# Kernel optimization log

Measured on AMD Instinct MI355X. Metric: run time of the kernel, lower is better.

The kernel has to match this reference:

```python
import jax, jax.numpy as jnp
import numpy as np

LN_EPS = 1e-9

def _layer_norm(x, g, b):
    mu = jnp.mean(x, axis=-1, keepdims=True)
    var = jnp.mean((x - mu) ** 2, axis=-1, keepdims=True)
    return (x - mu) * jax.lax.rsqrt(var + LN_EPS) * g + b

def _ffn(x, w1, b1, w2, b2, ln_g, ln_b):
    h = jax.nn.gelu(x @ w1 + b1, approximate=False)
    h = h @ w2 + b2
    return _layer_norm(h, ln_g, ln_b)

def _kernel_mean(x, y):
    d = x.shape[1]
    x2 = jnp.sum(x * x, axis=1)[:, None]
    y2 = jnp.sum(y * y, axis=1)[None, :]
    sq = x2 + y2 - 2.0 * (x @ y.T)  # [Nx, Ny]
    return jnp.mean(jnp.exp(-sq / (d * d)))

def _mmd(x, y):
    return _kernel_mean(x, x) + _kernel_mean(y, y) - 2.0 * _kernel_mean(x, y)

def setup_inputs() -> dict:
    key = jax.random.key(0)
    ks = jax.random.split(key, 8)
    B, S, D, DI, DL = 8, 512, 1024, 4096, 64
    s = lambda fan: 1.0 / np.sqrt(fan)
    return {
        "hidden": jax.random.normal(ks[0], (B, S, D), jnp.float32),
        "true_samples": jax.random.normal(ks[1], (B * S, DL), jnp.float32),
        "enc_w1": jax.random.normal(ks[2], (D, DI), jnp.float32) * s(D),
        "enc_b1": jnp.zeros((DI,), jnp.float32),
        "enc_w2": jax.random.normal(ks[3], (DI, DL), jnp.float32) * s(DI),
        "enc_b2": jnp.zeros((DL,), jnp.float32),
        "enc_ln_g": jnp.ones((DL,), jnp.float32),
        "enc_ln_b": jnp.zeros((DL,), jnp.float32),
        "dec_w1": jax.random.normal(ks[4], (DL, DI), jnp.float32) * s(DL),
        "dec_b1": jnp.zeros((DI,), jnp.float32),
        "dec_w2": jax.random.normal(ks[5], (DI, D), jnp.float32) * s(DI),
        "dec_b2": jnp.zeros((D,), jnp.float32),
        "dec_ln_g": jnp.ones((D,), jnp.float32),
        "dec_ln_b": jnp.zeros((D,), jnp.float32),
    }

def reference(hidden, true_samples, enc_w1, enc_b1, enc_w2, enc_b2, enc_ln_g, enc_ln_b,
              dec_w1, dec_b1, dec_w2, dec_b2, dec_ln_g, dec_ln_b):
    latent = _ffn(hidden, enc_w1, enc_b1, enc_w2, enc_b2, enc_ln_g, enc_ln_b)  # [B,S,DL]
    recon = _ffn(latent, dec_w1, dec_b1, dec_w2, dec_b2, dec_ln_g, dec_ln_b)   # [B,S,D]
    B, S, DL = latent.shape
    lat_flat = latent.reshape(-1, DL)  # [B*S, DL]
    reg_loss = _mmd(true_samples, lat_flat) / B * S
    return recon, latent, reg_loss
```

## Files before the change

### kernel.cpp

```cpp
#include <hip/hip_runtime.h>
#include <hip/hip_bf16.h>
#include <math.h>


typedef __attribute__((ext_vector_type(8))) short short8;
typedef __attribute__((ext_vector_type(4))) float float4a;
typedef __attribute__((ext_vector_type(4))) unsigned short us4;

__device__ inline ushort bf16r(float x) {
    union { float f; unsigned u; } c; c.f = x;
    unsigned r = (c.u + 0x7fffu + ((c.u >> 16) & 1u)) >> 16;
    return (ushort)r;
}

__device__ inline void gld_lds16(const void* g, void* l) {
    __builtin_amdgcn_global_load_lds(
        (const __attribute__((address_space(1))) void*)g,
        (__attribute__((address_space(3))) void*)l, 16, 0, 0);
}

template <int N> __device__ inline void wait_vmcnt() {
    if constexpr (N == 0) asm volatile("s_waitcnt vmcnt(0)" ::: "memory");
    else if constexpr (N == 4) asm volatile("s_waitcnt vmcnt(4)" ::: "memory");
    else if constexpr (N == 6) asm volatile("s_waitcnt vmcnt(6)" ::: "memory");
}

template <int N> __device__ inline void wait_lgkmcnt() {
    if constexpr (N == 0) asm volatile("s_waitcnt lgkmcnt(0)" ::: "memory");
    else if constexpr (N == 2) asm volatile("s_waitcnt lgkmcnt(2)" ::: "memory");
    else if constexpr (N == 4) asm volatile("s_waitcnt lgkmcnt(4)" ::: "memory");
    else if constexpr (N == 6) asm volatile("s_waitcnt lgkmcnt(6)" ::: "memory");
    else if constexpr (N == 8) asm volatile("s_waitcnt lgkmcnt(8)" ::: "memory");
}

__device__ inline void wait_lgkm_dyn(int n) {
    if (n == 0) wait_lgkmcnt<0>();
    else if (n == 2) wait_lgkmcnt<2>();
    else if (n == 4) wait_lgkmcnt<4>();
    else if (n == 6) wait_lgkmcnt<6>();
    else wait_lgkmcnt<8>();
}

__device__ inline float fast_gelu(float v) {
    float v2 = v * v;
    float u = v * __builtin_fmaf(0.07135481627f, v2, 1.5957691216f);
    u = fminf(u, 30.0f);
    float e = __expf(u);
    return v * e * __builtin_amdgcn_rcpf(e + 1.0f);
}

__global__ __launch_bounds__(256) void k_pre(
        const float* __restrict__ hidden, ushort* __restrict__ A1bf,
        const float* __restrict__ tsamp, ushort* __restrict__ Tbf,
        float* __restrict__ sq_t, float* __restrict__ acc,
        const float* __restrict__ i0, ushort* __restrict__ o0,
        const float* __restrict__ i1, ushort* __restrict__ o1,
        const float* __restrict__ i2, ushort* __restrict__ o2,
        const float* __restrict__ i3, ushort* __restrict__ o3) {
    int b = blockIdx.x, tid = threadIdx.x;
    if (b == 0 && tid < 24) acc[tid] = 0.0f;
    if (b < 4096) {
        int i = b * 1024 + tid * 4;
        float4 v = *(const float4*)(hidden + i);
        us4 o = {bf16r(v.x), bf16r(v.y), bf16r(v.z), bf16r(v.w)};
        *(us4*)(A1bf + i) = o;
        return;
    }
    if (b < 4352) {
        int i = (b - 4096) * 1024 + tid * 4;
        float4 v = *(const float4*)(tsamp + i);
        us4 o = {bf16r(v.x), bf16r(v.y), bf16r(v.z), bf16r(v.w)};
        *(us4*)(Tbf + i) = o;
        float s = v.x * v.x + v.y * v.y + v.z * v.z + v.w * v.w;
#pragma unroll
        for (int off = 8; off; off >>= 1) s += __shfl_xor(s, off);
        if ((tid & 15) == 0) sq_t[i >> 6] = s;
        return;
    }
    __shared__ float t[32][33];
    const float* in; ushort* out; int R, C, lb;
    if (b < 8448)      { in = i0; out = o0; R = 1024; C = 4096; lb = b - 4352; }
    else if (b < 8704) { in = i1; out = o1; R = 4096; C = 64;   lb = b - 8448; }
    else if (b < 8960) { in = i2; out = o2; R = 64;   C = 4096; lb = b - 8704; }
    else               { in = i3; out = o3; R = 4096; C = 1024; lb = b - 8960; }
    int bx = (lb % (C / 32)) * 32;
    int by = (lb / (C / 32)) * 32;
    int tx = tid & 31, ty = tid >> 5;
#pragma unroll
    for (int i = 0; i < 32; i += 8)
        t[ty + i][tx] = in[(size_t)(by + ty + i) * C + (bx + tx)];
    __syncthreads();
#pragma unroll
    for (int i = 0; i < 32; i += 8)
        out[(size_t)(bx + ty + i) * R + (by + tx)] = bf16r(t[tx][ty + i]);
}

template <int BN, int EPI, bool SWZ>
__global__ __launch_bounds__(256) void k_gemm(
        const ushort* __restrict__ A, const ushort* __restrict__ Bt,
        const float* __restrict__ bias, void* __restrict__ Out,
        float* __restrict__ Out2, int M, int N, int K, int KC) {
    constexpr int BM = 128, BK = 64;
    constexpr int WAVES_N = BN / 64;
    constexpr int WAVES_M = 4 / WAVES_N;
    constexpr int WM = BM / WAVES_M;
    constexpr int MT = WM / 16;
    constexpr int NT = 4;
    constexpr int CA = BM / 32, CB = BN / 32;

    __shared__ ushort sA[BM * 64];
    __shared__ ushort sB[BN * 64];

    const int tid  = threadIdx.x;
    const int wave = tid >> 6, lane = tid & 63;
    const int wm = wave / WAVES_N, wn = wave % WAVES_N;
    int bx = blockIdx.x, by = blockIdx.y;
    if constexpr (SWZ) {
        int lin = blockIdx.x + gridDim.x * blockIdx.y;
        by = lin % gridDim.y;
        bx = lin / gridDim.y;
    }
    const int m0 = by * BM, n0 = bx * BN;
    const int lrow = lane & 15, lq = lane >> 4;
    const int srow8 = lane >> 3;
    const int sk8   = lane & 7;
    const int kbeg = blockIdx.z * KC;

    const ushort* pA[CA]; unsigned lA[CA];
#pragma unroll
    for (int j = 0; j < CA; ++j) {
        int c = wave * CA + j;
        int r = c * 8 + srow8;
        pA[j] = &A[(size_t)(m0 + r) * K + kbeg + ((sk8 ^ (r & 7)) * 8)];
        lA[j] = c * 512;
    }
    const ushort* pB[CB]; unsigned lB[CB];
#pragma unroll
    for (int j = 0; j < CB; ++j) {
        int c = wave * CB + j;
        int r = c * 8 + srow8;
        pB[j] = &Bt[(size_t)(n0 + r) * K + kbeg + ((sk8 ^ (r & 7)) * 8)];
        lB[j] = c * 512;
    }
    unsigned aoff[2][MT], boff[2][NT];
#pragma unroll
    for (int h = 0; h < 2; ++h) {
#pragma unroll
        for (int mt = 0; mt < MT; ++mt) {
            int r = wm * WM + mt * 16 + lrow;
            aoff[h][mt] = r * 64 + (((h * 4 + lq) ^ (r & 7)) * 8);
        }
#pragma unroll
        for (int nt = 0; nt < NT; ++nt) {
            int r = wn * 64 + nt * 16 + lrow;
            boff[h][nt] = r * 64 + (((h * 4 + lq) ^ (r & 7)) * 8);
        }
    }

    float4a acc[MT][NT];
#pragma unroll
    for (int mt = 0; mt < MT; ++mt)
#pragma unroll
        for (int nt = 0; nt < NT; ++nt)
            acc[mt][nt] = (float4a){0.f, 0.f, 0.f, 0.f};

    for (int k0 = 0; k0 < KC; k0 += BK) {
#pragma unroll
        for (int j = 0; j < CA; ++j) {
            gld_lds16(pA[j], &sA[lA[j]]);
            pA[j] += BK;
        }
#pragma unroll
        for (int j = 0; j < CB; ++j) {
            gld_lds16(pB[j], &sB[lB[j]]);
            pB[j] += BK;
        }
        __syncthreads();
#pragma unroll
        for (int h = 0; h < 2; ++h) {
            short8 af[MT], bfr[NT];
#pragma unroll
            for (int mt = 0; mt < MT; ++mt)
                af[mt] = *(short8*)(&sA[aoff[h][mt]]);
#pragma unroll
            for (int nt = 0; nt < NT; ++nt)
                bfr[nt] = *(short8*)(&sB[boff[h][nt]]);
#pragma unroll
            for (int mt = 0; mt < MT; ++mt)
#pragma unroll
                for (int nt = 0; nt < NT; ++nt)
                    acc[mt][nt] = __builtin_amdgcn_mfma_f32_16x16x32_bf16(
                        af[mt], bfr[nt], acc[mt][nt], 0, 0, 0);
        }
        __syncthreads();
    }

    float* dstp = nullptr;
    if constexpr (EPI == 2) {
        if (Out2 && blockIdx.z) dstp = Out2;
        else dstp = (float*)Out + (size_t)blockIdx.z * M * N;
    }
#pragma unroll
    for (int mt = 0; mt < MT; ++mt)
#pragma unroll
        for (int nt = 0; nt < NT; ++nt) {
            int col = n0 + wn * 64 + nt * 16 + lrow;
            float bv = 0.f;
            if constexpr (EPI != 2) bv = bias[col];
#pragma unroll
            for (int r = 0; r < 4; ++r) {
                int row = m0 + wm * WM + mt * 16 + lq * 4 + r;
                float v = acc[mt][nt][r] + bv;
                if constexpr (EPI == 0) {
                    ((ushort*)Out)[(size_t)row * N + col] = bf16r(fast_gelu(v));
                } else if constexpr (EPI == 1) {
                    ((float*)Out)[(size_t)row * N + col] = v;
                } else {
                    dstp[(size_t)row * N + col] = v;
                }
            }
        }
}

template <int BN, int EPI, int CX, int CY>
__global__ __launch_bounds__(512, 2) void k_gemm256(
        const ushort* __restrict__ A, const ushort* __restrict__ Bt,
        const float* __restrict__ bias, void* __restrict__ Out,
        float* __restrict__ Out2, int M, int N, int K, int KC) {
    constexpr int BM = 256, BK = 64;
    constexpr int AI = 4;
    constexpr int BI = BN / 64;
    constexpr int WAVES_N = BN / 64;
    constexpr int WAVES_M = 8 / WAVES_N;
    constexpr int WM = BM / WAVES_M;
    constexpr int MT = WM / 16;
    constexpr int NT = 4;
    constexpr int NS = MT;
    constexpr int NS2 = MT / 2;

    __shared__ ushort sA[2][BM * 64];
    __shared__ ushort sB[2][BN * 64];

    const int tid = threadIdx.x;
    const int wave = tid >> 6, lane = tid & 63;
    const int wm = wave / WAVES_N, wn = wave % WAVES_N;

    const int gx = gridDim.x, gy = gridDim.y;
    const int lin = blockIdx.x + gx * (blockIdx.y + gy * blockIdx.z);
    const int nwg = gx * gy * gridDim.z;
    const int cpx = nwg >> 3;
    const int swz = (lin & 7) * cpx + (lin >> 3);
    const int nz  = gx * gy;
    const int zz  = swz / nz;
    const int rr  = swz % nz;
    const int chunk = rr / (CX * CY);
    const int lcl   = rr % (CX * CY);
    const int ncx   = gx / CX;
    const int bx = (chunk % ncx) * CX + (lcl % CX);
    const int by = (chunk / ncx) * CY + (lcl / CX);

    const int m0 = by * BM, n0 = bx * BN;
    const int lrow = lane & 15, lq = lane >> 4;
    const int kbeg = zz * KC;
    const int nT = KC / BK;

    const int crow = tid >> 3;
    const int ck8  = (tid & 7) ^ (crow & 7);
    const ushort* pAbase = A  + (size_t)(m0 + crow) * K + kbeg + ck8 * 8;
    const ushort* pBbase = Bt + (size_t)(n0 + crow) * K + kbeg + ck8 * 8;

    const int a0  = (wm * WM + lrow) * 64;
    const int b0  = (wn * 64 + lrow) * 64;
    const int sw0 = ((lq) ^ (lrow & 7)) * 8;
    const int sw1 = ((4 + lq) ^ (lrow & 7)) * 8;

    float4a acc[MT][NT];
#pragma unroll
    for (int mt = 0; mt < MT; ++mt)
#pragma unroll
        for (int nt = 0; nt < NT; ++nt)
            acc[mt][nt] = (float4a){0.f, 0.f, 0.f, 0.f};

#pragma unroll
    for (int j = 0; j < AI; ++j)
        gld_lds16(pAbase + (size_t)j * 64 * K, &sA[0][j * 4096 + wave * 512]);
#pragma unroll
    for (int j = 0; j < BI; ++j)
        gld_lds16(pBbase + (size_t)j * 64 * K, &sB[0][j * 4096 + wave * 512]);
    wait_vmcnt<0>();
    __builtin_amdgcn_s_barrier();
    __builtin_amdgcn_sched_barrier(0);

    for (int t = 0; t < nT; ++t) {
        const int d = t & 1;
        const bool pf1 = (t + 1 < nT);
        const size_t koff1 = (size_t)(t + 1) * BK;

        short8 af[NS][2], bfr[2][NT];

#pragma unroll
        for (int nt = 0; nt < NT; ++nt)
            bfr[0][nt] = *(const short8*)(&sB[d][b0 + nt * 1024 + sw0]);
        af[0][0] = *(const short8*)(&sA[d][a0 + 0 * 1024 + sw0]);
        af[0][1] = *(const short8*)(&sA[d][a0 + 1 * 1024 + sw0]);
        __builtin_amdgcn_sched_barrier(0);
        af[1][0] = *(const short8*)(&sA[d][a0 + 2 * 1024 + sw0]);
        af[1][1] = *(const short8*)(&sA[d][a0 + 3 * 1024 + sw0]);
        __builtin_amdgcn_sched_barrier(0);
        if (pf1) {
#pragma unroll
            for (int j = 0; j < AI; ++j)
                gld_lds16(pAbase + (size_t)j * 64 * K + koff1,
                          &sA[d ^ 1][j * 4096 + wave * 512]);
#pragma unroll
            for (int j = 0; j < BI; ++j)
                gld_lds16(pBbase + (size_t)j * 64 * K + koff1,
                          &sB[d ^ 1][j * 4096 + wave * 512]);
        }
        __builtin_amdgcn_sched_barrier(0);

#pragma unroll
        for (int s = 0; s < NS; ++s) {
            const int s2 = s + 2;
            if (s2 < NS) {
                const int h2 = s2 / NS2;
                const int mb2 = (s2 % NS2) * 2;
                const int swh2 = h2 ? sw1 : sw0;
                if ((s2 % NS2) == 0) {
#pragma unroll
                    for (int nt = 0; nt < NT; ++nt)
                        bfr[h2][nt] =
                            *(const short8*)(&sB[d][b0 + nt * 1024 + swh2]);
                }
                af[s2][0] = *(const short8*)(&sA[d][a0 + (mb2 + 0) * 1024 + swh2]);
                af[s2][1] = *(const short8*)(&sA[d][a0 + (mb2 + 1) * 1024 + swh2]);
                __builtin_amdgcn_sched_barrier(0);
            }
            int Ns = 0;
            if (s + 1 < NS) Ns += (((s + 1) % NS2) == 0) ? (2 + NT) : 2;
            if (s + 2 < NS) Ns += (((s + 2) % NS2) == 0) ? (2 + NT) : 2;
            wait_lgkm_dyn(Ns);
            __builtin_amdgcn_sched_barrier(0);
            const int h = s / NS2, mb = (s % NS2) * 2;
            __builtin_amdgcn_s_setprio(1);
#pragma unroll
            for (int i = 0; i < 2; ++i)
#pragma unroll
                for (int nt = 0; nt < NT; ++nt)
                    acc[mb + i][nt] = __builtin_amdgcn_mfma_f32_16x16x32_bf16(
                        af[s][i], bfr[h][nt], acc[mb + i][nt], 0, 0, 0);
            __builtin_amdgcn_s_setprio(0);
        }
        if (pf1) {
            wait_vmcnt<0>();
            __builtin_amdgcn_s_barrier();
            __builtin_amdgcn_sched_barrier(0);
        }
    }

    float* dstp = nullptr;
    if constexpr (EPI == 2) {
        if (Out2 && zz) dstp = Out2;
        else dstp = (float*)Out + (size_t)zz * M * N;
    }
#pragma unroll
    for (int mt = 0; mt < MT; ++mt)
#pragma unroll
        for (int nt = 0; nt < NT; ++nt) {
            const int col = n0 + wn * 64 + nt * 16 + lrow;
            float bv = 0.f;
            if constexpr (EPI == 0) bv = bias[col];
#pragma unroll
            for (int r = 0; r < 4; ++r) {
                const int row = m0 + wm * WM + mt * 16 + lq * 4 + r;
                float v = acc[mt][nt][r] + bv;
                if constexpr (EPI == 0)
                    ((ushort*)Out)[(size_t)row * N + col] = bf16r(fast_gelu(v));
                else
                    dstp[(size_t)row * N + col] = v;
            }
        }
}

__global__ __launch_bounds__(256) void k_gram_all(
        const ushort* __restrict__ Tbf, const ushort* __restrict__ Lbf,
        const float* __restrict__ sq_t, const float* __restrict__ sq_l,
        float* __restrict__ accum) {
    __shared__ ushort sX[128 * 64];
    __shared__ ushort sY[128 * 64];
    __shared__ float red[4];

    int id = blockIdx.x;
    int pair, tbx, tby; float w;
    if (id < 1056) {
        pair = (id < 528) ? 0 : 1;
        int t = (pair == 0) ? id : id - 528;
        int r = (int)((sqrtf(8.0f * t + 1.0f) - 1.0f) * 0.5f);
        while ((r + 1) * (r + 2) / 2 <= t) ++r;
        while (r * (r + 1) / 2 > t) --r;
        tby = r; tbx = t - r * (r + 1) / 2;
        w = (tbx == tby) ? 1.0f : 2.0f;
    } else {
        pair = 2; int t = id - 1056;
        tbx = t & 31; tby = t >> 5; w = 1.0f;
    }
    const ushort* Xb = (pair == 1) ? Lbf : Tbf;
    const ushort* Yb = (pair == 0) ? Tbf : Lbf;
    const float* sqX = (pair == 1) ? sq_l : sq_t;
    const float* sqY = (pair == 0) ? sq_t : sq_l;

    const int tid  = threadIdx.x;
    const int wave = tid >> 6, lane = tid & 63;
    const int wm = wave >> 1, wn = wave & 1;
    const int bx = tbx * 128, by = tby * 128;
    const int lrow = lane & 15, lq = lane >> 4;
    const int srow8 = lane >> 3, sk8 = lane & 7;

#pragma unroll
    for (int j = 0; j < 4; ++j) {
        int c = wave * 4 + j;
        int r = c * 8 + srow8;
        int kc = (sk8 ^ (r & 7)) * 8;
        gld_lds16(&Xb[(size_t)(bx + r) * 64 + kc], &sX[c * 512]);
        gld_lds16(&Yb[(size_t)(by + r) * 64 + kc], &sY[c * 512]);
    }

    unsigned xoff[2][4], yoff[2][4];
#pragma unroll
    for (int h = 0; h < 2; ++h)
#pragma unroll
        for (int i = 0; i < 4; ++i) {
            int rx = wm * 64 + i * 16 + lrow;
            int ry = wn * 64 + i * 16 + lrow;
            xoff[h][i] = rx * 64 + (((h * 4 + lq) ^ (rx & 7)) * 8);
            yoff[h][i] = ry * 64 + (((h * 4 + lq) ^ (ry & 7)) * 8);
        }
    __syncthreads();

    float4a acc[4][4];
#pragma unroll
    for (int mt = 0; mt < 4; ++mt)
#pragma unroll
        for (int nt = 0; nt < 4; ++nt)
            acc[mt][nt] = (float4a){0.f, 0.f, 0.f, 0.f};

#pragma unroll
    for (int h = 0; h < 2; ++h) {
        short8 xf[4], yf[4];
#pragma unroll
        for (int mt = 0; mt < 4; ++mt)
            xf[mt] = *(short8*)(&sX[xoff[h][mt]]);
#pragma unroll
        for (int nt = 0; nt < 4; ++nt)
            yf[nt] = *(short8*)(&sY[yoff[h][nt]]);
#pragma unroll
        for (int mt = 0; mt < 4; ++mt)
#pragma unroll
            for (int nt = 0; nt < 4; ++nt)
                acc[mt][nt] = __builtin_amdgcn_mfma_f32_16x16x32_bf16(
                    xf[mt], yf[nt], acc[mt][nt], 0, 0, 0);
    }

    float sy[4];
#pragma unroll
    for (int nt = 0; nt < 4; ++nt)
        sy[nt] = sqY[by + wn * 64 + nt * 16 + lrow];
    float s = 0.f;
#pragma unroll
    for (int mt = 0; mt < 4; ++mt)
#pragma unroll
        for (int r = 0; r < 4; ++r) {
            float sx = sqX[bx + wm * 64 + mt * 16 + lq * 4 + r];
#pragma unroll
            for (int nt = 0; nt < 4; ++nt)
                s += __expf((2.0f * acc[mt][nt][r] - sx - sy[nt]) * (1.0f / 4096.0f));
        }
    s *= w;
#pragma unroll
    for (int off = 32; off; off >>= 1) s += __shfl_xor(s, off);
    if ((tid & 63) == 0) red[tid >> 6] = s;
    __syncthreads();
    if (tid == 0) atomicAdd(accum + pair * 8, red[0] + red[1] + red[2] + red[3]);
}

__global__ __launch_bounds__(256) void k_ln64_red(
        const float* __restrict__ part, int npart,
        const float* __restrict__ bias, const float* __restrict__ g,
        const float* __restrict__ b, float* __restrict__ outf,
        ushort* __restrict__ outb, float* __restrict__ sq_l) {
    int wave = threadIdx.x >> 6, lane = threadIdx.x & 63;
    int row = blockIdx.x * 4 + wave;
    float x = bias[lane];
    for (int s = 0; s < npart; ++s)
        x += part[(size_t)s * 4096 * 64 + row * 64 + lane];
    float s = x;
#pragma unroll
    for (int off = 32; off; off >>= 1) s += __shfl_xor(s, off);
    float mu = s * (1.0f / 64.0f);
    float d = x - mu;
    float v = d * d;
#pragma unroll
    for (int off = 32; off; off >>= 1) v += __shfl_xor(v, off);
    float rs = rsqrtf(v * (1.0f / 64.0f) + 1e-9f);
    float y = d * rs * g[lane] + b[lane];
    outf[row * 64 + lane] = y;
    outb[row * 64 + lane] = bf16r(y);
    float q = y * y;
#pragma unroll
    for (int off = 32; off; off >>= 1) q += __shfl_xor(q, off);
    if (lane == 0) sq_l[row] = q;
}

__global__ __launch_bounds__(256) void k_ln1024_red(
        const float* __restrict__ p0, const float* __restrict__ p1,
        const float* __restrict__ bias, const float* __restrict__ g,
        const float* __restrict__ b, float* __restrict__ out) {
    __shared__ float red[4];
    int row = blockIdx.x, tid = threadIdx.x;
    const float4 v0 = *(const float4*)(p0 + (size_t)row * 1024 + tid * 4);
    const float4 v1 = *(const float4*)(p1 + (size_t)row * 1024 + tid * 4);
    const float4 bb = *(const float4*)(bias + tid * 4);
    float4 v;
    v.x = v0.x + v1.x + bb.x;
    v.y = v0.y + v1.y + bb.y;
    v.z = v0.z + v1.z + bb.z;
    v.w = v0.w + v1.w + bb.w;
    float s = v.x + v.y + v.z + v.w;
#pragma unroll
    for (int off = 32; off; off >>= 1) s += __shfl_xor(s, off);
    if ((tid & 63) == 0) red[tid >> 6] = s;
    __syncthreads();
    float mu = (red[0] + red[1] + red[2] + red[3]) * (1.0f / 1024.0f);
    float dx = v.x - mu, dy = v.y - mu, dz = v.z - mu, dw = v.w - mu;
    float q = dx * dx + dy * dy + dz * dz + dw * dw;
#pragma unroll
    for (int off = 32; off; off >>= 1) q += __shfl_xor(q, off);
    __syncthreads();
    if ((tid & 63) == 0) red[tid >> 6] = q;
    __syncthreads();
    float rs = rsqrtf((red[0] + red[1] + red[2] + red[3]) * (1.0f / 1024.0f) + 1e-9f);
    const float4 gv = *(const float4*)(g + tid * 4);
    const float4 bv = *(const float4*)(b + tid * 4);
    float4 o;
    o.x = dx * rs * gv.x + bv.x;
    o.y = dy * rs * gv.y + bv.y;
    o.z = dz * rs * gv.z + bv.z;
    o.w = dw * rs * gv.w + bv.w;
    *(float4*)(out + (size_t)row * 1024 + tid * 4) = o;
}

__global__ void k_finalize(const float* __restrict__ accum, float* __restrict__ out) {
    out[0] = (accum[0] + accum[8] - 2.0f * accum[16]) * (64.0f / (4096.0f * 4096.0f));
}

extern "C" void kernel_launch(void* const* d_in, const int* in_sizes, int n_in,
                              void* d_out, int out_size, void* d_ws, size_t ws_size,
                              hipStream_t stream) {
    const float* hidden   = (const float*)d_in[0];
    const float* tsamp    = (const float*)d_in[1];
    const float* enc_w1   = (const float*)d_in[2];
    const float* enc_b1   = (const float*)d_in[3];
    const float* enc_w2   = (const float*)d_in[4];
    const float* enc_b2   = (const float*)d_in[5];
    const float* enc_ln_g = (const float*)d_in[6];
    const float* enc_ln_b = (const float*)d_in[7];
    const float* dec_w1   = (const float*)d_in[8];
    const float* dec_b1   = (const float*)d_in[9];
    const float* dec_w2   = (const float*)d_in[10];
    const float* dec_b2   = (const float*)d_in[11];
    const float* dec_ln_g = (const float*)d_in[12];
    const float* dec_ln_b = (const float*)d_in[13];

    float* out      = (float*)d_out;
    float* recon    = out;
    float* latent_f = out + 4194304;
    float* reg      = out + 4456448;

    char* ws = (char*)d_ws;
    const size_t MB = 1024 * 1024;
    ushort* A1bf = (ushort*)(ws + 0);
    ushort* W1t  = (ushort*)(ws + 8 * MB);
    float*  part = (float*)(ws + 0);
    float*  h4p0 = (float*)(ws + 0);
    ushort* H1bf = (ushort*)(ws + 16 * MB);
    ushort* W4t  = (ushort*)(ws + 48 * MB);
    ushort* W2t  = (ushort*)(ws + 56 * MB);
    ushort* W3t  = (ushort*)(ws + 56 * MB + 512 * 1024);
    ushort* Lbf  = (ushort*)(ws + 57 * MB);
    float*  sq_t = (float*)(ws + 59 * MB);
    float*  sq_l = (float*)(ws + 59 * MB + 16384);
    float*  acc3 = (float*)(ws + 59 * MB + 32768);
    ushort* Tbf  = (ushort*)(ws + 59 * MB + 65536);

    k_pre<<<13056, 256, 0, stream>>>(hidden, A1bf, tsamp, Tbf, sq_t, acc3,
                                     enc_w1, W1t, enc_w2, W2t,
                                     dec_w1, W3t, dec_w2, W4t);

    k_gemm256<128, 0, 8, 4><<<dim3(32, 16, 1), 512, 0, stream>>>(
        A1bf, W1t, enc_b1, H1bf, nullptr, 4096, 4096, 1024, 1024);
    k_gemm<64, 2, false><<<dim3(1, 32, 16), 256, 0, stream>>>(
        H1bf, W2t, nullptr, part, nullptr, 4096, 64, 4096, 256);
    k_ln64_red<<<1024, 256, 0, stream>>>(part, 16, enc_b2, enc_ln_g, enc_ln_b,
                                         latent_f, Lbf, sq_l);

    k_gemm<64, 0, false><<<dim3(64, 32, 1), 256, 0, stream>>>(
        Lbf, W3t, dec_b1, H1bf, nullptr, 4096, 4096, 64, 64);
    k_gemm256<128, 2, 8, 4><<<dim3(8, 16, 2), 512, 0, stream>>>(
        H1bf, W4t, nullptr, h4p0, recon, 4096, 1024, 4096, 2048);
    k_ln1024_red<<<4096, 256, 0, stream>>>(h4p0, recon, dec_b2, dec_ln_g,
                                           dec_ln_b, recon);

    k_gram_all<<<2080, 256, 0, stream>>>(Tbf, Lbf, sq_t, sq_l, acc3);
    k_finalize<<<1, 1, 0, stream>>>(acc3, reg);
}
```

Before: 281.4 us.

## Add 256x256 double-buffered GEMM for encoder layer, widen transpose tiles

Adds a new k_gemm256mb kernel with 256x256 tiles, double-buffered LDS and split k-half fragment loads overlapped with MFMA. It is used for the first encoder GEMM in place of the 256x128 variant, which halves the grid and raises data reuse per block. The weight-transpose pre-kernel now handles 64x32 tiles with packed ushort2 stores, so it needs fewer blocks. The larger tile puts more pressure on registers and LDS and may lower occupancy.

```diff
diff --git a/kernel.cpp b/kernel.cpp
--- a/kernel.cpp
+++ b/kernel.cpp
@@ -31,6 +31,7 @@
     else if constexpr (N == 4) asm volatile("s_waitcnt lgkmcnt(4)" ::: "memory");
     else if constexpr (N == 6) asm volatile("s_waitcnt lgkmcnt(6)" ::: "memory");
     else if constexpr (N == 8) asm volatile("s_waitcnt lgkmcnt(8)" ::: "memory");
+    else if constexpr (N == 12) asm volatile("s_waitcnt lgkmcnt(12)" ::: "memory");
 }
 
 __device__ inline void wait_lgkm_dyn(int n) {
@@ -77,22 +78,28 @@
         if ((tid & 15) == 0) sq_t[i >> 6] = s;
         return;
     }
-    __shared__ float t[32][33];
-    const float* in; ushort* out; int R, C, lb;
-    if (b < 8448)      { in = i0; out = o0; R = 1024; C = 4096; lb = b - 4352; }
-    else if (b < 8704) { in = i1; out = o1; R = 4096; C = 64;   lb = b - 8448; }
-    else if (b < 8960) { in = i2; out = o2; R = 64;   C = 4096; lb = b - 8704; }
-    else               { in = i3; out = o3; R = 4096; C = 1024; lb = b - 8960; }
+    __shared__ float t[32][65];
+    const float* in; ushort* out; int R, C;
+    int lb = b - 4352;
+    if (lb < 2048)      { in = i0; out = o0; R = 1024; C = 4096; }
+    else if (lb < 2176) { in = i1; out = o1; R = 4096; C = 64;   lb -= 2048; }
+    else if (lb < 2304) { in = i2; out = o2; R = 64;   C = 4096; lb -= 2176; }
+    else                { in = i3; out = o3; R = 4096; C = 1024; lb -= 2304; }
     int bx = (lb % (C / 32)) * 32;
-    int by = (lb / (C / 32)) * 32;
+    int by = (lb / (C / 32)) * 64;
     int tx = tid & 31, ty = tid >> 5;
 #pragma unroll
-    for (int i = 0; i < 32; i += 8)
-        t[ty + i][tx] = in[(size_t)(by + ty + i) * C + (bx + tx)];
+    for (int i = 0; i < 64; i += 8)
+        t[tx][i + ty] = in[(size_t)(by + i + ty) * C + (bx + tx)];
     __syncthreads();
 #pragma unroll
-    for (int i = 0; i < 32; i += 8)
-        out[(size_t)(bx + ty + i) * R + (by + tx)] = bf16r(t[tx][ty + i]);
+    for (int i = 0; i < 32; i += 8) {
+        int c = i + ty;
+        ushort2 o;
+        o.x = bf16r(t[c][2 * tx]);
+        o.y = bf16r(t[c][2 * tx + 1]);
+        *(ushort2*)(&out[(size_t)(bx + c) * R + by + 2 * tx]) = o;
+    }
 }
 
 template <int BN, int EPI, bool SWZ>
@@ -223,7 +230,154 @@
 }
 
 template <int BN, int EPI, int CX, int CY>
-__global__ __launch_bounds__(512, 2) void k_gemm256(
+__global__ __launch_bounds__(512, 2) void k_gemm256mb(
+        const ushort* __restrict__ A, const ushort* __restrict__ Bt,
+        const float* __restrict__ bias, void* __restrict__ Out,
+        float* __restrict__ Out2, int M, int N, int K, int KC) {
+    constexpr int BM = 256, BK = 64;
+    constexpr int AI = 4;
+    constexpr int BI = BN / 64;
+    constexpr int WAVES_N = BN / 64;
+    constexpr int WAVES_M = 8 / WAVES_N;
+    constexpr int WM = BM / WAVES_M;
+    constexpr int MT = WM / 16;
+    constexpr int NT = 4;
+
+    __shared__ ushort sA[2][BM * 64];
+    __shared__ ushort sB[2][BN * 64];
+
+    const int tid = threadIdx.x;
+    const int wave = tid >> 6, lane = tid & 63;
+    const int wm = wave / WAVES_N, wn = wave % WAVES_N;
+
+    const int gx = gridDim.x, gy = gridDim.y;
+    const int lin = blockIdx.x + gx * (blockIdx.y + gy * blockIdx.z);
+    const int nwg = gx * gy * gridDim.z;
+    const int cpx = nwg >> 3;
+    const int swz = (lin & 7) * cpx + (lin >> 3);
+    const int nz  = gx * gy;
+    const int zz  = swz / nz;
+    const int rr  = swz % nz;
+    const int chunk = rr / (CX * CY);
+    const int lcl   = rr % (CX * CY);
+    const int ncx   = gx / CX;
+    const int bx = (chunk % ncx) * CX + (lcl % CX);
+    const int by = (chunk / ncx) * CY + (lcl / CX);
+
+    const int m0 = by * BM, n0 = bx * BN;
+    const int lrow = lane & 15, lq = lane >> 4;
+    const int kbeg = zz * KC;
+    const int nT = KC / BK;
+
+    const int crow = tid >> 3;
+    const int ck8  = (tid & 7) ^ (crow & 7);
+    const ushort* pAbase = A  + (size_t)(m0 + crow) * K + kbeg + ck8 * 8;
+    const ushort* pBbase = Bt + (size_t)(n0 + crow) * K + kbeg + ck8 * 8;
+
+    const int a0  = (wm * WM + lrow) * 64;
+    const int b0  = (wn * 64 + lrow) * 64;
+    const int sw0 = ((lq) ^ (lrow & 7)) * 8;
+    const int sw1 = ((4 + lq) ^ (lrow & 7)) * 8;
+
+    float4a acc[MT][NT];
+#pragma unroll
+    for (int mt = 0; mt < MT; ++mt)
+#pragma unroll
+        for (int nt = 0; nt < NT; ++nt)
+            acc[mt][nt] = (float4a){0.f, 0.f, 0.f, 0.f};
+
+#pragma unroll
+    for (int j = 0; j < AI; ++j)
+        gld_lds16(pAbase + (size_t)j * 64 * K, &sA[0][j * 4096 + wave * 512]);
+#pragma unroll
+    for (int j = 0; j < BI; ++j)
+        gld_lds16(pBbase + (size_t)j * 64 * K, &sB[0][j * 4096 + wave * 512]);
+    wait_vmcnt<0>();
+    __builtin_amdgcn_s_barrier();
+    __builtin_amdgcn_sched_barrier(0);
+
+    for (int t = 0; t < nT; ++t) {
+        const int d = t & 1;
+        const bool pf1 = (t + 1 < nT);
+        const size_t koff1 = (size_t)(t + 1) * BK;
+
+        short8 af0[MT], bfr0[NT], af1[MT], bfr1[NT];
+#pragma unroll
+        for (int mt = 0; mt < MT; ++mt)
+            af0[mt] = *(const short8*)(&sA[d][a0 + mt * 1024 + sw0]);
+#pragma unroll
+        for (int nt = 0; nt < NT; ++nt)
+            bfr0[nt] = *(const short8*)(&sB[d][b0 + nt * 1024 + sw0]);
+        __builtin_amdgcn_sched_barrier(0);
+#pragma unroll
+        for (int mt = 0; mt < MT; ++mt)
+            af1[mt] = *(const short8*)(&sA[d][a0 + mt * 1024 + sw1]);
+#pragma unroll
+        for (int nt = 0; nt < NT; ++nt)
+            bfr1[nt] = *(const short8*)(&sB[d][b0 + nt * 1024 + sw1]);
+        if (pf1) {
+#pragma unroll
+            for (int j = 0; j < AI; ++j)
+                gld_lds16(pAbase + (size_t)j * 64 * K + koff1,
+                          &sA[d ^ 1][j * 4096 + wave * 512]);
+#pragma unroll
+            for (int j = 0; j < BI; ++j)
+                gld_lds16(pBbase + (size_t)j * 64 * K + koff1,
+                          &sB[d ^ 1][j * 4096 + wave * 512]);
+        }
+        wait_lgkmcnt<MT + 4>();
+        __builtin_amdgcn_sched_barrier(0);
+        __builtin_amdgcn_s_setprio(1);
+#pragma unroll
+        for (int mt = 0; mt < MT; ++mt)
+#pragma unroll
+            for (int nt = 0; nt < NT; ++nt)
+                acc[mt][nt] = __builtin_amdgcn_mfma_f32_16x16x32_bf16(
+                    af0[mt], bfr0[nt], acc[mt][nt], 0, 0, 0);
+        __builtin_amdgcn_s_setprio(0);
+        wait_lgkmcnt<0>();
+        __builtin_amdgcn_sched_barrier(0);
+        __builtin_amdgcn_s_setprio(1);
+#pragma unroll
+        for (int mt = 0; mt < MT; ++mt)
+#pragma unroll
+            for (int nt = 0; nt < NT; ++nt)
+                acc[mt][nt] = __builtin_amdgcn_mfma_f32_16x16x32_bf16(
+                    af1[mt], bfr1[nt], acc[mt][nt], 0, 0, 0);
+        __builtin_amdgcn_s_setprio(0);
+        if (pf1) {
+            wait_vmcnt<0>();
+            __builtin_amdgcn_s_barrier();
+            __builtin_amdgcn_sched_barrier(0);
+        }
+    }
+
+    float* dstp = nullptr;
+    if constexpr (EPI == 2) {
+        if (Out2 && zz) dstp = Out2;
+        else dstp = (float*)Out + (size_t)zz * M * N;
+    }
+#pragma unroll
+    for (int mt = 0; mt < MT; ++mt)
+#pragma unroll
+        for (int nt = 0; nt < NT; ++nt) {
+            const int col = n0 + wn * 64 + nt * 16 + lrow;
+            float bv = 0.f;
+            if constexpr (EPI == 0) bv = bias[col];
+#pragma unroll
+            for (int r = 0; r < 4; ++r) {
+                const int row = m0 + wm * WM + mt * 16 + lq * 4 + r;
+                float v = acc[mt][nt][r] + bv;
+                if constexpr (EPI == 0)
+                    ((ushort*)Out)[(size_t)row * N + col] = bf16r(fast_gelu(v));
+                else
+                    dstp[(size_t)row * N + col] = v;
+            }
+        }
+}
+
+template <int BN, int EPI, int CX, int CY>
+__global__ __launch_bounds__(512, 2) void k_gemm256sp(
         const ushort* __restrict__ A, const ushort* __restrict__ Bt,
         const float* __restrict__ bias, void* __restrict__ Out,
         float* __restrict__ Out2, int M, int N, int K, int KC) {
@@ -592,11 +746,11 @@
     float*  acc3 = (float*)(ws + 59 * MB + 32768);
     ushort* Tbf  = (ushort*)(ws + 59 * MB + 65536);
 
-    k_pre<<<13056, 256, 0, stream>>>(hidden, A1bf, tsamp, Tbf, sq_t, acc3,
-                                     enc_w1, W1t, enc_w2, W2t,
-                                     dec_w1, W3t, dec_w2, W4t);
-
-    k_gemm256<128, 0, 8, 4><<<dim3(32, 16, 1), 512, 0, stream>>>(
+    k_pre<<<8704, 256, 0, stream>>>(hidden, A1bf, tsamp, Tbf, sq_t, acc3,
+                                    enc_w1, W1t, enc_w2, W2t,
+                                    dec_w1, W3t, dec_w2, W4t);
+
+    k_gemm256mb<256, 0, 4, 8><<<dim3(16, 16, 1), 512, 0, stream>>>(
         A1bf, W1t, enc_b1, H1bf, nullptr, 4096, 4096, 1024, 1024);
     k_gemm<64, 2, false><<<dim3(1, 32, 16), 256, 0, stream>>>(
         H1bf, W2t, nullptr, part, nullptr, 4096, 64, 4096, 256);
@@ -605,7 +759,7 @@
 
     k_gemm<64, 0, false><<<dim3(64, 32, 1), 256, 0, stream>>>(
         Lbf, W3t, dec_b1, H1bf, nullptr, 4096, 4096, 64, 64);
-    k_gemm256<128, 2, 8, 4><<<dim3(8, 16, 2), 512, 0, stream>>>(
+    k_gemm256sp<128, 2, 8, 4><<<dim3(8, 16, 2), 512, 0, stream>>>(
         H1bf, W4t, nullptr, h4p0, recon, 4096, 1024, 4096, 2048);
     k_ln1024_red<<<4096, 256, 0, stream>>>(h4p0, recon, dec_b2, dec_ln_g,
                                            dec_ln_b, recon);
```

New measurement: 270.1 us. 1.04x faster.
